# Performance work log

Measured on AMD Instinct MI355X. Metric: run time of the kernel, lower is better.

Reference implementation:

```python
import jax, jax.numpy as jnp
import numpy as np

B, S, C, H, L = 256, 8, 8, 501, 56


def _lin_init(k, out_dim, in_dim):
    k1, k2 = jax.random.split(k)
    s = 1.0 / np.sqrt(in_dim)
    w = jax.random.uniform(k1, (out_dim, in_dim), jnp.float32, -s, s)
    b = jax.random.uniform(k2, (out_dim,), jnp.float32, -s, s)
    return w, b


def setup_inputs() -> dict:
    key = jax.random.key(0)
    ks = jax.random.split(key, 12)
    lin1_w, lin1_b = _lin_init(ks[0], H, L)
    av_w1, av_b1 = _lin_init(ks[1], 2 * H, H)
    av_w2, av_b2 = _lin_init(ks[2], C, 2 * H)
    ae_w1, ae_b1 = _lin_init(ks[3], 4 * H, 2 * H)
    ae_w2, ae_b2 = _lin_init(ks[4], 1, 4 * H)
    gate_w, gate_b = _lin_init(ks[5], H, H)
    map_w, map_b = _lin_init(ks[6], H, H)
    gru_w_ih, gru_b_ih = _lin_init(ks[7], 3 * H, C)
    gru_w_hh, gru_b_hh = _lin_init(ks[8], 3 * H, H)
    z = jax.random.normal(ks[9], (B, L), jnp.float32)
    dep_graph = jax.random.uniform(ks[10], (B, S, S), jnp.float32)
    node_encoding = jax.random.uniform(ks[11], (B, S, C), jnp.float32)
    return dict(z=z, dep_graph=dep_graph, node_encoding=node_encoding,
                lin1_w=lin1_w, lin1_b=lin1_b,
                av_w1=av_w1, av_b1=av_b1, av_w2=av_w2, av_b2=av_b2,
                ae_w1=ae_w1, ae_b1=ae_b1, ae_w2=ae_w2, ae_b2=ae_b2,
                gate_w=gate_w, gate_b=gate_b, map_w=map_w, map_b=map_b,
                gru_w_ih=gru_w_ih, gru_w_hh=gru_w_hh,
                gru_b_ih=gru_b_ih, gru_b_hh=gru_b_hh)


def _forward(z, dep_graph, node_encoding,
             lin1_w, lin1_b, av_w1, av_b1, av_w2, av_b2,
             ae_w1, ae_b1, ae_w2, ae_b2, gate_w, gate_b, map_w, map_b,
             gru_w_ih, gru_w_hh, gru_b_ih, gru_b_hh):
    b, s, _ = dep_graph.shape
    h = lin1_w.shape[0]

    def gru(x, hid):  # torch GRUCell math
        gi = x @ gru_w_ih.T + gru_b_ih
        gh = hid @ gru_w_hh.T + gru_b_hh
        i_r, i_z, i_n = jnp.split(gi, 3, axis=-1)
        h_r, h_z, h_n = jnp.split(gh, 3, axis=-1)
        r = jax.nn.sigmoid(i_r + h_r)
        zz = jax.nn.sigmoid(i_z + h_z)
        n = jnp.tanh(i_n + r * h_n)
        return (1.0 - zz) * n + zz * hid

    pos = jnp.arange(s)

    def outer_step(carry, xs):
        graph_state, nhs = carry  # (B,H), (B,S,H)
        index, x, dep_row = xs    # scalar, (B,C), (B,S)
        logits = jax.nn.softmax(
            jax.nn.relu(graph_state @ av_w1.T + av_b1) @ av_w2.T + av_b2, axis=-1)
        # index==0: gru seeded with graph_state; otherwise zero hidden
        h0 = jnp.where(index == 0, graph_state, jnp.zeros_like(graph_state))
        hv0 = gru(x, h0)

        def inner_step(c, j):
            hv, nhs_c, edge_row = c
            active = j < index  # replicate range(index-1, -1, -1)
            hidden_j = nhs_c[:, j]
            e = jnp.concatenate([hv, hidden_j], axis=1)
            edge = (jax.nn.relu(e @ ae_w1.T + ae_b1) @ ae_w2.T + ae_b2)[:, 0]
            edge_row = edge_row.at[:, j].set(jnp.where(active, edge, 0.0))
            # ancestors: dep_graph[:, index] with positions < j zeroed
            anc = dep_row * (pos >= j).astype(dep_row.dtype)
            a = (nhs_c * anc[:, :, None]).reshape(b * s, h)
            h_in = (jax.nn.sigmoid(a @ gate_w.T + gate_b) *
                    (a @ map_w.T + map_b)).reshape(b, s, h).sum(axis=1)
            hv_new = gru(x, h_in)
            hv = jnp.where(active, hv_new, hv)
            nhs_c = nhs_c.at[:, index].set(jnp.where(active, hv_new, nhs_c[:, index]))
            return (hv, nhs_c, edge_row), None

        (hv, nhs, edge_row), _ = jax.lax.scan(
            inner_step, (hv0, nhs, jnp.zeros((b, s), dep_graph.dtype)),
            jnp.arange(s - 1, -1, -1))
        nhs = nhs.at[:, index].set(hv)
        return (hv, nhs), (logits, edge_row)

    graph_state0 = z @ lin1_w.T + lin1_b
    nhs0 = jnp.zeros((b, s, h), z.dtype)
    (_, _), (gen_enc, gen_dep) = jax.lax.scan(
        outer_step, (graph_state0, nhs0),
        (jnp.arange(s), node_encoding.transpose(1, 0, 2), dep_graph.transpose(1, 0, 2)))
    return gen_dep.transpose(1, 0, 2), gen_enc.transpose(1, 0, 2)


def reference(z, dep_graph, node_encoding,
              lin1_w, lin1_b, av_w1, av_b1, av_w2, av_b2,
              ae_w1, ae_b1, ae_w2, ae_b2, gate_w, gate_b, map_w, map_b,
              gru_w_ih, gru_w_hh, gru_b_ih, gru_b_hh):
    return _forward(z, dep_graph, node_encoding,
                    lin1_w, lin1_b, av_w1, av_b1, av_w2, av_b2,
                    ae_w1, ae_b1, ae_w2, ae_b2, gate_w, gate_b, map_w, map_b,
                    gru_w_ih, gru_w_hh, gru_b_ih, gru_b_hh)
```

## Files before the change

kernel.cpp:

```cpp
#include <hip/hip_runtime.h>
#include <math.h>

constexpr int NB  = 256;
constexpr int NS  = 8;
constexpr int NC  = 8;
constexpr int NH  = 501;
constexpr int NL  = 56;
constexpr int NH2 = 1002;
constexpr int NH3 = 1503;
constexpr int NH4 = 2004;
constexpr int KT  = 1536;
constexpr int KE  = 512;
constexpr int KA  = 1024;
constexpr int HV  = 512 * 256;

typedef unsigned short u16;
typedef short bf16x8v __attribute__((ext_vector_type(8)));
typedef _Float16 f16x8v __attribute__((ext_vector_type(8)));
typedef _Float16 f16x4v __attribute__((ext_vector_type(4)));
typedef float f32x4 __attribute__((ext_vector_type(4)));

__device__ __forceinline__ float sigf(float x) { return 1.0f / (1.0f + __expf(-x)); }
__device__ __forceinline__ float tanh2(float x) { return 2.0f * sigf(2.0f * x) - 1.0f; }

__device__ __forceinline__ u16 f2bf(float x) {
  union { float f; unsigned u; } c; c.f = x;
  unsigned r = (c.u + 0x7fffu + ((c.u >> 16) & 1u)) >> 16;
  return (u16)r;
}
__device__ __forceinline__ float bf2f(u16 h) {
  union { float f; unsigned u; } c; c.u = ((unsigned)h) << 16; return c.f;
}

__device__ __forceinline__ void async_copy16(const void* g, void* l) {
  __builtin_amdgcn_global_load_lds(
      (const __attribute__((address_space(1))) unsigned int*)g,
      (__attribute__((address_space(3))) unsigned int*)l, 16, 0, 0);
}

__device__ __forceinline__ f32x4 mfma_bf(bf16x8v a, bf16x8v b, f32x4 c) {
  return __builtin_amdgcn_mfma_f32_16x16x32_bf16(a, b, c, 0, 0, 0);
}
__device__ __forceinline__ f32x4 mfma_h(f16x8v a, f16x8v b, f32x4 c) {
  return __builtin_amdgcn_mfma_f32_16x16x32_f16(a, b, c, 0, 0, 0);
}

__device__ __forceinline__ void storeTrio(u16* __restrict__ T, int b, int h0, const float v[4]) {
  size_t base = (size_t)b * KT;
  if (h0 + 3 < NH) {
    ushort4 hi4, lo4;
    u16 hi, lo;
    hi = f2bf(v[0]); lo = f2bf(v[0] - bf2f(hi)); hi4.x = hi; lo4.x = lo;
    hi = f2bf(v[1]); lo = f2bf(v[1] - bf2f(hi)); hi4.y = hi; lo4.y = lo;
    hi = f2bf(v[2]); lo = f2bf(v[2] - bf2f(hi)); hi4.z = hi; lo4.z = lo;
    hi = f2bf(v[3]); lo = f2bf(v[3] - bf2f(hi)); hi4.w = hi; lo4.w = lo;
    *(ushort4*)&T[base + h0]        = hi4;
    *(ushort4*)&T[base + 512 + h0]  = lo4;
    *(ushort4*)&T[base + 1024 + h0] = hi4;
  } else {
    for (int r = 0; r < 4; ++r) {
      int h = h0 + r;
      if (h < NH) {
        u16 hi = f2bf(v[r]); u16 lo = f2bf(v[r] - bf2f(hi));
        T[base + h] = hi; T[base + 512 + h] = lo; T[base + 1024 + h] = hi;
      }
    }
  }
}

__global__ __launch_bounds__(256) void kPack(
    const float* __restrict__ gate_w, const float* __restrict__ map_w,
    const float* __restrict__ w_hh, const float* __restrict__ av_w1,
    const float* __restrict__ ae_w1,
    u16* __restrict__ Wgm, u16* __restrict__ Whh, u16* __restrict__ Wav1,
    _Float16* __restrict__ Wlr) {
  int r = blockIdx.x;
  if (r < 3584) {
    for (int k = threadIdx.x; k < 512; k += 256) {
      float v = 0.f; u16* dst; int rr;
      if (r < 1024) {
        int h = (r < 512) ? r : r - 512;
        if (h < NH && k < NH) v = (r < 512) ? gate_w[h * NH + k] : map_w[h * NH + k];
        dst = Wgm; rr = r;
      } else if (r < 2560) {
        rr = r - 1024; int g = rr >> 9, h = rr & 511;
        if (h < NH && k < NH) v = w_hh[((size_t)g * NH + h) * NH + k];
        dst = Whh;
      } else {
        rr = r - 2560;
        if (rr < NH2 && k < NH) v = av_w1[(size_t)rr * NH + k];
        dst = Wav1;
      }
      u16 hi = f2bf(v); u16 lo = f2bf(v - bf2f(hi));
      dst[(size_t)rr * KT + k] = hi;
      dst[(size_t)rr * KT + 512 + k] = hi;
      dst[(size_t)rr * KT + 1024 + k] = lo;
    }
  } else {
    int m = r - 3584;
    for (int k = threadIdx.x; k < KA; k += 256) {
      float v = 0.f;
      if (m < NH4) {
        if (k < 512) { if (k < NH) v = ae_w1[(size_t)m * NH2 + k]; }
        else { int kk = k - 512; if (kk < NH) v = ae_w1[(size_t)m * NH2 + NH + kk]; }
      }
      Wlr[(size_t)m * KA + k] = (_Float16)v;
    }
  }
}

__global__ __launch_bounds__(256) void kInit(
    float* __restrict__ out0, const float* __restrict__ ae_b2,
    u16* __restrict__ trio, _Float16* __restrict__ Xe, _Float16* __restrict__ Xn,
    const float* __restrict__ z, const float* __restrict__ lin1_w,
    const float* __restrict__ lin1_b, float* __restrict__ g0,
    const float* __restrict__ ne, const float* __restrict__ w_ih,
    const float* __restrict__ b_ih, float* __restrict__ giN, float* __restrict__ giT) {
  int blk = blockIdx.x, t = threadIdx.x;
  if (blk < 64) {
    int e = blk * 256 + t;
    int b = e >> 6, r = e & 63;
    int i = r >> 3, jj = r & 7;
    out0[b * 64 + i * 8 + jj] = (jj < i) ? ae_b2[0] : 0.f;
  } else if (blk < 75) {
    u16* T = trio + (size_t)(blk - 64) * ((size_t)NB * KT) + (size_t)t * KT;
#pragma unroll
    for (int seg = 0; seg < 3; ++seg)
      for (int h = NH; h < 512; ++h) T[seg * 512 + h] = 0;
  } else if (blk < 103) {
    _Float16* X = Xe + (size_t)(blk - 75) * NB * KE + (size_t)t * KE;
    for (int h = NH; h < 512; ++h) X[h] = (_Float16)0.f;
  } else if (blk < 110) {
    _Float16* X = Xn + (size_t)(blk - 103) * NB * KE + (size_t)t * KE;
    for (int h = NH; h < 512; ++h) X[h] = (_Float16)0.f;
  } else if (blk < 366) {
    int b = blk - 110;
    const float* zr = z + (size_t)b * NL;
    for (int h = t; h < NH; h += 256) {
      const float* wr = lin1_w + (size_t)h * NL;
      float acc = lin1_b[h];
#pragma unroll
      for (int l = 0; l < NL; ++l) acc += zr[l] * wr[l];
      g0[h * NB + b] = acc;
      u16 hi = f2bf(acc), lo = f2bf(acc - bf2f(hi));
      trio[(size_t)b * KT + h] = hi;
      trio[(size_t)b * KT + 512 + h] = lo;
      trio[(size_t)b * KT + 1024 + h] = hi;
    }
  } else {
    int r0 = (blk - 366) * 6, b = t;
    for (int rr = 0; rr < 6; ++rr) {
      int r = r0 + rr;
      if (r >= NH3) break;
      int g = (r >= NH2) ? 2 : ((r >= NH) ? 1 : 0);
      int h = r - g * NH;
      float wv[8];
#pragma unroll
      for (int c = 0; c < 8; ++c) wv[c] = w_ih[r * NC + c];
      float bb = b_ih[r];
      for (int idx = 0; idx < 8; ++idx) {
        float acc = bb;
#pragma unroll
        for (int c = 0; c < 8; ++c) acc += ne[b * 64 + idx * 8 + c] * wv[c];
        giN[((size_t)idx * NH3 + r) * NB + b] = acc;
        giT[((size_t)idx * NB + b) * KT + g * 512 + h] = acc;
      }
    }
  }
}


__global__ __launch_bounds__(256) void kGMT(
    const u16* __restrict__ Wgm, const u16* __restrict__ Bsrc,
    float* __restrict__ PcO, float* __restrict__ QcO,
    const float* __restrict__ dep, const float* __restrict__ gate_b,
    const float* __restrict__ map_b, float* __restrict__ RS, u16* __restrict__ hinT,
    const float* __restrict__ giT, const float* __restrict__ b_hh,
    _Float16* __restrict__ Xe0, int index) {
  __shared__ f32x4 red[4 * 4 * 64];
  const int b = blockIdx.x, t = threadIdx.x, w = t >> 6, l = t & 63;
  const int quad = l >> 4, lan = l & 15;
  const int ht = b & 31, ct = b >> 5;
  const u16* Ag = Wgm + (size_t)(ht * 16 + lan) * KT;
  const u16* Am = Wgm + (size_t)(512 + ht * 16 + lan) * KT;
  const u16* B0 = Bsrc + (size_t)(ct * 32 + lan) * KT;
  const u16* B1 = Bsrc + (size_t)(ct * 32 + 16 + lan) * KT;
  const int kb = w * 384 + quad * 8;
  f32x4 a0 = {0.f,0.f,0.f,0.f}, a1 = a0, a2 = a0, a3 = a0;
#pragma unroll 4
  for (int ks = 0; ks < 12; ++ks) {
    int k = kb + ks * 32;
    bf16x8v bg = *(const bf16x8v*)&B0[k];
    bf16x8v bh = *(const bf16x8v*)&B1[k];
    bf16x8v ag = *(const bf16x8v*)&Ag[k];
    bf16x8v am = *(const bf16x8v*)&Am[k];
    a0 = mfma_bf(ag, bg, a0); a1 = mfma_bf(ag, bh, a1);
    a2 = mfma_bf(am, bg, a2); a3 = mfma_bf(am, bh, a3);
  }
  red[(w * 4 + 0) * 64 + l] = a0;
  red[(w * 4 + 1) * 64 + l] = a1;
  red[(w * 4 + 2) * 64 + l] = a2;
  red[(w * 4 + 3) * 64 + l] = a3;
  __syncthreads();
  if (w < 2) {
    int ns = w;
    f32x4 G = red[(0 * 4 + ns) * 64 + l] + red[(1 * 4 + ns) * 64 + l] +
              red[(2 * 4 + ns) * 64 + l] + red[(3 * 4 + ns) * 64 + l];
    f32x4 M = red[(0 * 4 + 2 + ns) * 64 + l] + red[(1 * 4 + 2 + ns) * 64 + l] +
              red[(2 * 4 + 2 + ns) * 64 + l] + red[(3 * 4 + 2 + ns) * 64 + l];
    int c = ct * 32 + ns * 16 + lan;
    int h0 = ht * 16 + quad * 4;
    int j = index - 1;
    float dj = dep[c * 64 + index * 8 + j];
    float vout[4];
#pragma unroll
    for (int reg = 0; reg < 4; ++reg) {
      int h = h0 + reg; float v = 0.f;
      if (h < NH) {
        PcO[h * NB + c] = G[reg];
        QcO[h * NB + c] = M[reg];
        float gb = gate_b[h], mb = map_b[h];
        float kbv = sigf(gb) * mb;
        float fj = sigf(dj * G[reg] + gb) * (dj * M[reg] + mb);
        RS[h * NB + c] = fj;
        v = fj + 7.0f * kbv;
      }
      vout[reg] = v;
    }
    storeTrio(hinT, c, h0, vout);
  } else {
    int t2 = t - 128;
    int c = ct * 32 + (t2 & 31);
    int hb = t2 >> 5;
    const float* g = giT + ((size_t)index * NB + c) * KT;
#pragma unroll
    for (int k = 0; k < 4; ++k) {
      int h = ht * 16 + hb * 4 + k;
      if (h < NH) {
        float rr = sigf(g[h] + b_hh[h]);
        float zz = sigf(g[512 + h] + b_hh[NH + h]);
        float nn = tanh2(g[1024 + h] + rr * b_hh[2 * NH + h]);
        Xe0[(size_t)c * KE + h] = (_Float16)((1.f - zz) * nn);
      }
    }
  }
}

__global__ __launch_bounds__(256) void kGM0(
    const u16* __restrict__ Wgm, const u16* __restrict__ Bsrc,
    const float* __restrict__ dep, const float* __restrict__ gate_b,
    const float* __restrict__ map_b,
    const float* __restrict__ Pcj, const float* __restrict__ Qcj,
    float* __restrict__ RS, u16* __restrict__ hinT, int index, int j) {
  __shared__ f32x4 red[4 * 4 * 64];
  const int b = blockIdx.x, t = threadIdx.x, w = t >> 6, l = t & 63;
  const int quad = l >> 4, lan = l & 15;
  const int ht = b & 31, ct = b >> 5;
  const u16* Ag = Wgm + (size_t)(ht * 16 + lan) * KT;
  const u16* Am = Wgm + (size_t)(512 + ht * 16 + lan) * KT;
  const u16* B0 = Bsrc + (size_t)(ct * 32 + lan) * KT;
  const u16* B1 = Bsrc + (size_t)(ct * 32 + 16 + lan) * KT;
  const int kb = w * 384 + quad * 8;
  f32x4 a0 = {0.f,0.f,0.f,0.f}, a1 = a0, a2 = a0, a3 = a0;
#pragma unroll 4
  for (int ks = 0; ks < 12; ++ks) {
    int k = kb + ks * 32;
    bf16x8v bg = *(const bf16x8v*)&B0[k];
    bf16x8v bh = *(const bf16x8v*)&B1[k];
    bf16x8v ag = *(const bf16x8v*)&Ag[k];
    bf16x8v am = *(const bf16x8v*)&Am[k];
    a0 = mfma_bf(ag, bg, a0); a1 = mfma_bf(ag, bh, a1);
    a2 = mfma_bf(am, bg, a2); a3 = mfma_bf(am, bh, a3);
  }
  red[(w * 4 + 0) * 64 + l] = a0;
  red[(w * 4 + 1) * 64 + l] = a1;
  red[(w * 4 + 2) * 64 + l] = a2;
  red[(w * 4 + 3) * 64 + l] = a3;
  __syncthreads();
  if (w < 2) {
    int ns = w;
    f32x4 G = red[(0 * 4 + ns) * 64 + l] + red[(1 * 4 + ns) * 64 + l] +
              red[(2 * 4 + ns) * 64 + l] + red[(3 * 4 + ns) * 64 + l];
    f32x4 M = red[(0 * 4 + 2 + ns) * 64 + l] + red[(1 * 4 + 2 + ns) * 64 + l] +
              red[(2 * 4 + 2 + ns) * 64 + l] + red[(3 * 4 + 2 + ns) * 64 + l];
    int c = ct * 32 + ns * 16 + lan;
    int h0 = ht * 16 + quad * 4;
    float dj = dep[c * 64 + index * 8 + j];
    float di = dep[c * 64 + index * 8 + index];
    float cnt = (float)(7 - (index - j));
    float vout[4];
#pragma unroll
    for (int reg = 0; reg < 4; ++reg) {
      int h = h0 + reg; float v = 0.f;
      if (h < NH) {
        float gb = gate_b[h], mb = map_b[h];
        float kbv = sigf(gb) * mb;
        float fj = sigf(dj * Pcj[h * NB + c] + gb) * (dj * Qcj[h * NB + c] + mb);
        float rs = RS[h * NB + c] + fj;
        RS[h * NB + c] = rs;
        float fi = sigf(di * G[reg] + gb) * (di * M[reg] + mb);
        v = rs + fi + cnt * kbv;
      }
      vout[reg] = v;
    }
    storeTrio(hinT, c, h0, vout);
  }
}

__global__ __launch_bounds__(256) void kHHw(
    const u16* __restrict__ Whh, const u16* __restrict__ Bsrc,
    const float* __restrict__ hidF, const float* __restrict__ gi,
    const float* __restrict__ b_hh,
    u16* __restrict__ dstT, _Float16* __restrict__ XeSlot, _Float16* __restrict__ XnSlot) {
  __shared__ f32x4 red[4 * 6 * 64];
  const int b = blockIdx.x, t = threadIdx.x, w = t >> 6, l = t & 63;
  const int quad = l >> 4, lan = l & 15;
  const int ht = b & 31, ct = b >> 5;
  const u16* Ar = Whh + (size_t)(ht * 16 + lan) * KT;
  const u16* Az = Whh + (size_t)(512 + ht * 16 + lan) * KT;
  const u16* An = Whh + (size_t)(1024 + ht * 16 + lan) * KT;
  const u16* B0 = Bsrc + (size_t)(ct * 32 + lan) * KT;
  const u16* B1 = Bsrc + (size_t)(ct * 32 + 16 + lan) * KT;
  const int kb = w * 384 + quad * 8;
  f32x4 r0 = {0.f,0.f,0.f,0.f}, r1 = r0, z0 = r0, z1 = r0, n0 = r0, n1 = r0;
#pragma unroll 4
  for (int ks = 0; ks < 12; ++ks) {
    int k = kb + ks * 32;
    bf16x8v bg = *(const bf16x8v*)&B0[k];
    bf16x8v bh = *(const bf16x8v*)&B1[k];
    bf16x8v ar = *(const bf16x8v*)&Ar[k];
    bf16x8v az = *(const bf16x8v*)&Az[k];
    bf16x8v an = *(const bf16x8v*)&An[k];
    r0 = mfma_bf(ar, bg, r0); r1 = mfma_bf(ar, bh, r1);
    z0 = mfma_bf(az, bg, z0); z1 = mfma_bf(az, bh, z1);
    n0 = mfma_bf(an, bg, n0); n1 = mfma_bf(an, bh, n1);
  }
  red[(w * 6 + 0) * 64 + l] = r0;
  red[(w * 6 + 1) * 64 + l] = r1;
  red[(w * 6 + 2) * 64 + l] = z0;
  red[(w * 6 + 3) * 64 + l] = z1;
  red[(w * 6 + 4) * 64 + l] = n0;
  red[(w * 6 + 5) * 64 + l] = n1;
  __syncthreads();
  if (w < 2) {
    int ns = w;
    f32x4 Rr = red[(0 * 6 + 0 + ns) * 64 + l] + red[(1 * 6 + 0 + ns) * 64 + l] +
               red[(2 * 6 + 0 + ns) * 64 + l] + red[(3 * 6 + 0 + ns) * 64 + l];
    f32x4 Rz = red[(0 * 6 + 2 + ns) * 64 + l] + red[(1 * 6 + 2 + ns) * 64 + l] +
               red[(2 * 6 + 2 + ns) * 64 + l] + red[(3 * 6 + 2 + ns) * 64 + l];
    f32x4 Rn = red[(0 * 6 + 4 + ns) * 64 + l] + red[(1 * 6 + 4 + ns) * 64 + l] +
               red[(2 * 6 + 4 + ns) * 64 + l] + red[(3 * 6 + 4 + ns) * 64 + l];
    int c = ct * 32 + ns * 16 + lan;
    int h0 = ht * 16 + quad * 4;
    float vout[4];
#pragma unroll
    for (int reg = 0; reg < 4; ++reg) {
      int h = h0 + reg; float v = 0.f;
      if (h < NH) {
        float ir = gi[h * NB + c];
        float iz = gi[(NH + h) * NB + c];
        float inn = gi[(2 * NH + h) * NB + c];
        float rr = sigf(ir + Rr[reg] + b_hh[h]);
        float zz = sigf(iz + Rz[reg] + b_hh[NH + h]);
        float nn = tanh2(inn + rr * (Rn[reg] + b_hh[2 * NH + h]));
        float hd;
        if (hidF) hd = hidF[h * NB + c];
        else hd = bf2f(Bsrc[(size_t)c * KT + h]) + bf2f(Bsrc[(size_t)c * KT + 512 + h]);
        v = (1.f - zz) * nn + zz * hd;
      }
      vout[reg] = v;
    }
    storeTrio(dstT, c, h0, vout);
    if (XeSlot || XnSlot) {
      if (h0 + 3 < NH) {
        f16x4v xv; xv[0] = (_Float16)vout[0]; xv[1] = (_Float16)vout[1];
        xv[2] = (_Float16)vout[2]; xv[3] = (_Float16)vout[3];
        if (XeSlot) *(f16x4v*)&XeSlot[(size_t)c * KE + h0] = xv;
        if (XnSlot) *(f16x4v*)&XnSlot[(size_t)c * KE + h0] = xv;
      } else {
        for (int reg = 0; reg < 4; ++reg)
          if (h0 + reg < NH) {
            if (XeSlot) XeSlot[(size_t)c * KE + h0 + reg] = (_Float16)vout[reg];
            if (XnSlot) XnSlot[(size_t)c * KE + h0 + reg] = (_Float16)vout[reg];
          }
      }
    }
  }
}


__global__ __launch_bounds__(256) void kEdge(const _Float16* __restrict__ Wlr,
                                             const _Float16* __restrict__ Xe,
                                             const _Float16* __restrict__ Xn,
                                             const float* __restrict__ ae_b1,
                                             const float* __restrict__ ae_w2,
                                             float* __restrict__ out0) {
  __shared__ u16 sA[2][128 * 32];
  __shared__ u16 sB[2][128 * 32];
  __shared__ float shW[4][8][16];
  const int t = threadIdx.x, w = t >> 6, l = t & 63, quad = l >> 4, lan = l & 15;
  const int mB = blockIdx.x * 128, nB0 = blockIdx.y * 128;
  const int qs = quad ^ ((lan >> 1) & 3);
  const int sseg = (l & 3) ^ ((l >> 3) & 3);
  int sid = blockIdx.y >> 1;
  int idec = 1, bse = 0;
  while (sid >= bse + idec) { bse += idec; idec++; }
  int jdec = idec - 1 - (sid - bse);
  int r0 = (w * 2 + 0) * 16 + (l >> 2), r1 = (w * 2 + 1) * 16 + (l >> 2);
  const _Float16* gA0 = Wlr + (size_t)(mB + r0) * KA + sseg * 8;
  const _Float16* gA1 = Wlr + (size_t)(mB + r1) * KA + sseg * 8;
  const _Float16* Xe0 = Xe + (size_t)(nB0 + r0) * KE + sseg * 8;
  const _Float16* Xe1 = Xe + (size_t)(nB0 + r1) * KE + sseg * 8;
  const _Float16* Xn0 = Xn + ((size_t)jdec * NB + ((nB0 + r0) & 255)) * KE + sseg * 8;
  const _Float16* Xn1 = Xn + ((size_t)jdec * NB + ((nB0 + r1) & 255)) * KE + sseg * 8;
  f32x4 acc[2][8];
#pragma unroll
  for (int mt = 0; mt < 2; ++mt)
#pragma unroll
    for (int ns = 0; ns < 8; ++ns) acc[mt][ns] = (f32x4){0.f,0.f,0.f,0.f};
  async_copy16(gA0, &sA[0][(w * 2 + 0) * 512]);
  async_copy16(gA1, &sA[0][(w * 2 + 1) * 512]);
  async_copy16(Xe0, &sB[0][(w * 2 + 0) * 512]);
  async_copy16(Xe1, &sB[0][(w * 2 + 1) * 512]);
  for (int c = 0; c < 32; ++c) {
    __syncthreads();
    if (c + 1 < 32) {
      int nb = (c + 1) & 1, cc = c + 1;
      async_copy16(gA0 + cc * 32, &sA[nb][(w * 2 + 0) * 512]);
      async_copy16(gA1 + cc * 32, &sA[nb][(w * 2 + 1) * 512]);
      const _Float16* b0 = (cc < 16) ? (Xe0 + cc * 32) : (Xn0 + (cc - 16) * 32);
      const _Float16* b1 = (cc < 16) ? (Xe1 + cc * 32) : (Xn1 + (cc - 16) * 32);
      async_copy16(b0, &sB[nb][(w * 2 + 0) * 512]);
      async_copy16(b1, &sB[nb][(w * 2 + 1) * 512]);
    }
    const u16* bufA = sA[c & 1];
    const u16* bufB = sB[c & 1];
    f16x8v av[2];
#pragma unroll
    for (int mt = 0; mt < 2; ++mt)
      av[mt] = *(const f16x8v*)&bufA[(w * 32 + mt * 16 + lan) * 32 + qs * 8];
#pragma unroll
    for (int ns = 0; ns < 8; ++ns) {
      f16x8v bv = *(const f16x8v*)&bufB[(ns * 16 + lan) * 32 + qs * 8];
#pragma unroll
      for (int mt = 0; mt < 2; ++mt) acc[mt][ns] = mfma_h(av[mt], bv, acc[mt][ns]);
    }
  }
  float b1v[2][4], w2v[2][4];
#pragma unroll
  for (int mt = 0; mt < 2; ++mt) {
    int m0 = mB + w * 32 + mt * 16 + quad * 4;
#pragma unroll
    for (int reg = 0; reg < 4; ++reg) {
      int m = m0 + reg;
      b1v[mt][reg] = (m < NH4) ? ae_b1[m] : 0.f;
      w2v[mt][reg] = (m < NH4) ? ae_w2[m] : 0.f;
    }
  }
#pragma unroll
  for (int ns = 0; ns < 8; ++ns) {
    float s = 0.f;
#pragma unroll
    for (int mt = 0; mt < 2; ++mt) {
#pragma unroll
      for (int reg = 0; reg < 4; ++reg) {
        float v = acc[mt][ns][reg] + b1v[mt][reg];
        if (v > 0.f) s += v * w2v[mt][reg];
      }
    }
    s += __shfl_xor(s, 16);
    s += __shfl_xor(s, 32);
    if (quad == 0) shW[w][ns][lan] = s;
  }
  __syncthreads();
  if (t < 128) {
    int ns = t >> 4, ln = t & 15;
    float tot = shW[0][ns][ln] + shW[1][ns][ln] + shW[2][ns][ln] + shW[3][ns][ln];
    int b = (nB0 + ln + ns * 16) & 255;
    atomicAdd(&out0[b * 64 + idec * 8 + jdec], tot);
  }
}

__global__ __launch_bounds__(256) void kLogA(const u16* __restrict__ Wav1,
                                             const u16* __restrict__ Bsrc,
                                             const float* __restrict__ av_b1,
                                             _Float16* __restrict__ t1) {
  __shared__ u16 sA[2][64 * 32];
  __shared__ u16 sB[2][128 * 32];
  const int t = threadIdx.x, w = t >> 6, l = t & 63, quad = l >> 4, lan = l & 15;
  const int mB = blockIdx.x * 64, nB0 = blockIdx.y * 128;
  const int qs = quad ^ ((lan >> 1) & 3);
  const int sseg = (l & 3) ^ ((l >> 3) & 3);
  int rA = w * 16 + (l >> 2);
  int r0 = (w * 2 + 0) * 16 + (l >> 2), r1 = (w * 2 + 1) * 16 + (l >> 2);
  const u16* gA = Wav1 + (size_t)(mB + rA) * KT + sseg * 8;
  const u16* gB0 = Bsrc + (size_t)(nB0 + r0) * KT + sseg * 8;
  const u16* gB1 = Bsrc + (size_t)(nB0 + r1) * KT + sseg * 8;
  f32x4 acc[8];
#pragma unroll
  for (int ns = 0; ns < 8; ++ns) acc[ns] = (f32x4){0.f,0.f,0.f,0.f};
  async_copy16(gA, &sA[0][w * 512]);
  async_copy16(gB0, &sB[0][(w * 2 + 0) * 512]);
  async_copy16(gB1, &sB[0][(w * 2 + 1) * 512]);
  for (int c = 0; c < 48; ++c) {
    __syncthreads();
    if (c + 1 < 48) {
      int nb = (c + 1) & 1, off = (c + 1) * 32;
      async_copy16(gA + off, &sA[nb][w * 512]);
      async_copy16(gB0 + off, &sB[nb][(w * 2 + 0) * 512]);
      async_copy16(gB1 + off, &sB[nb][(w * 2 + 1) * 512]);
    }
    const u16* bufA = sA[c & 1];
    const u16* bufB = sB[c & 1];
    bf16x8v av = *(const bf16x8v*)&bufA[(w * 16 + lan) * 32 + qs * 8];
#pragma unroll
    for (int ns = 0; ns < 8; ++ns) {
      bf16x8v bv = *(const bf16x8v*)&bufB[(ns * 16 + lan) * 32 + qs * 8];
      acc[ns] = mfma_bf(av, bv, acc[ns]);
    }
  }
#pragma unroll
  for (int ns = 0; ns < 8; ++ns) {
    int col = nB0 + ns * 16 + lan;
    int m0 = mB + w * 16 + quad * 4;
    f16x4v rv;
#pragma unroll
    for (int reg = 0; reg < 4; ++reg) {
      int m = m0 + reg;
      float v = acc[ns][reg] + ((m < NH2) ? av_b1[m] : 0.f);
      rv[reg] = (_Float16)(v > 0.f ? v : 0.f);
    }
    *(f16x4v*)&t1[(size_t)col * 1024 + m0] = rv;
  }
}

__global__ __launch_bounds__(256) void kSoft(const _Float16* __restrict__ t1,
                                             const float* __restrict__ av_w2,
                                             const float* __restrict__ av_b2,
                                             float* __restrict__ out1) {
  const int t = threadIdx.x, w = t >> 6, l = t & 63;
  int col = blockIdx.x * 4 + w;
  const _Float16* trow = t1 + (size_t)col * 1024;
  float s[8] = {};
  for (int i = 0; i < 16; ++i) {
    int k = i * 64 + l;
    if (k < NH2) {
      float v = (float)trow[k];
#pragma unroll
      for (int c = 0; c < 8; ++c) s[c] += v * av_w2[c * NH2 + k];
    }
  }
#pragma unroll
  for (int c = 0; c < 8; ++c) {
    s[c] += __shfl_xor(s[c], 32);
    s[c] += __shfl_xor(s[c], 16);
    s[c] += __shfl_xor(s[c], 8);
    s[c] += __shfl_xor(s[c], 4);
    s[c] += __shfl_xor(s[c], 2);
    s[c] += __shfl_xor(s[c], 1);
  }
  if (l == 0) {
    float lg[8], mx = -1e30f;
#pragma unroll
    for (int c = 0; c < 8; ++c) { lg[c] = s[c] + av_b2[c]; mx = fmaxf(mx, lg[c]); }
    float den = 0.f;
#pragma unroll
    for (int c = 0; c < 8; ++c) den += __expf(lg[c] - mx);
    int idx = col >> 8, b = col & 255;
#pragma unroll
    for (int c = 0; c < 8; ++c)
      out1[(b * NS + idx) * NC + c] = __expf(lg[c] - mx) / den;
  }
}


extern "C" void kernel_launch(void* const* d_in, const int* in_sizes, int n_in,
                              void* d_out, int out_size, void* d_ws, size_t ws_size,
                              hipStream_t stream) {
  (void)in_sizes; (void)n_in; (void)out_size; (void)ws_size;
  const float* z      = (const float*)d_in[0];
  const float* dep    = (const float*)d_in[1];
  const float* ne     = (const float*)d_in[2];
  const float* lin1_w = (const float*)d_in[3];
  const float* lin1_b = (const float*)d_in[4];
  const float* av_w1  = (const float*)d_in[5];
  const float* av_b1  = (const float*)d_in[6];
  const float* av_w2  = (const float*)d_in[7];
  const float* av_b2  = (const float*)d_in[8];
  const float* ae_w1  = (const float*)d_in[9];
  const float* ae_b1  = (const float*)d_in[10];
  const float* ae_w2  = (const float*)d_in[11];
  const float* ae_b2  = (const float*)d_in[12];
  const float* gate_w = (const float*)d_in[13];
  const float* gate_b = (const float*)d_in[14];
  const float* map_w  = (const float*)d_in[15];
  const float* map_b  = (const float*)d_in[16];
  const float* w_ih   = (const float*)d_in[17];
  const float* w_hh   = (const float*)d_in[18];
  const float* b_ih   = (const float*)d_in[19];
  const float* b_hh   = (const float*)d_in[20];

  float* out0 = (float*)d_out;
  float* out1 = out0 + NB * NS * NS;

  const size_t SLOT = (size_t)NB * KT;
  char* p = (char*)d_ws;
  u16* trio = (u16*)p;            p += 11 * SLOT * 2;
  _Float16* Xe = (_Float16*)p;    p += (size_t)28 * NB * KE * 2;
  _Float16* Xn = (_Float16*)p;    p += (size_t)7 * NB * KE * 2;
  u16* Wgm  = (u16*)p;            p += (size_t)1024 * KT * 2;
  u16* Whh  = (u16*)p;            p += (size_t)1536 * KT * 2;
  u16* Wav1 = (u16*)p;            p += (size_t)1024 * KT * 2;
  _Float16* Wlr = (_Float16*)p;   p += (size_t)2048 * KA * 2;
  _Float16* t1 = (_Float16*)p;    p += (size_t)2048 * 1024 * 2;
  float* Pc   = (float*)p;        p += (size_t)8 * HV * 4;
  float* Qc   = (float*)p;        p += (size_t)8 * HV * 4;
  float* RS   = (float*)p;        p += (size_t)HV * 4;
  float* g0   = (float*)p;        p += (size_t)HV * 4;
  float* giN  = (float*)p;        p += (size_t)8 * NH3 * NB * 4;
  float* giT  = (float*)p;        p += (size_t)8 * NB * KT * 4;

  u16* hinT = trio + 8 * SLOT;

  kPack<<<5632, 256, 0, stream>>>(gate_w, map_w, w_hh, av_w1, ae_w1, Wgm, Whh, Wav1, Wlr);
  kInit<<<617, 256, 0, stream>>>(out0, ae_b2, trio, Xe, Xn,
                                 z, lin1_w, lin1_b, g0, ne, w_ih, b_ih, giN, giT);

  kHHw<<<256, 256, 0, stream>>>(Whh, trio, g0, giN, b_hh,
                                trio + 1 * SLOT, nullptr, Xn);

  for (int i = 0; i <= 6; ++i) {
    int index = i + 1;
    int sid0 = index * (index - 1) / 2;
    const float* gi_i = giN + (size_t)index * NH3 * NB;
    kGMT<<<256, 256, 0, stream>>>(Wgm, trio + (size_t)(i + 1) * SLOT,
                                  Pc + (size_t)i * HV, Qc + (size_t)i * HV,
                                  dep, gate_b, map_b, RS, hinT, giT, b_hh,
                                  Xe + (size_t)sid0 * NB * KE, index);
    bool final1 = (index == 1);
    u16* dst = final1 ? (trio + 2 * SLOT) : (trio + 9 * SLOT);
    kHHw<<<256, 256, 0, stream>>>(Whh, hinT, nullptr, gi_i, b_hh, dst,
        (index - 1 > 0) ? (Xe + (size_t)(sid0 + 1) * NB * KE) : nullptr,
        final1 ? (Xn + (size_t)1 * NB * KE) : nullptr);
    u16* prev = dst;
    int par = 1;
    for (int j = index - 2; j >= 0; --j) {
      kGM0<<<256, 256, 0, stream>>>(Wgm, prev, dep, gate_b, map_b,
                                    Pc + (size_t)j * HV, Qc + (size_t)j * HV,
                                    RS, hinT, index, j);
      bool fin = (j == 0);
      u16* d2 = (fin && index <= 6) ? (trio + (size_t)(index + 1) * SLOT)
                                    : (trio + (size_t)(9 + par) * SLOT);
      kHHw<<<256, 256, 0, stream>>>(Whh, hinT, nullptr, gi_i, b_hh, d2,
          (j > 0) ? (Xe + (size_t)(sid0 + index - j) * NB * KE) : nullptr,
          (fin && index <= 6) ? (Xn + (size_t)index * NB * KE) : nullptr);
      prev = d2; par ^= 1;
    }
  }

  kLogA<<<dim3(16, 16), 256, 0, stream>>>(Wav1, trio, av_b1, t1);
  kSoft<<<512, 256, 0, stream>>>(t1, av_w2, av_b2, out1);
  kEdge<<<dim3(16, 56), 256, 0, stream>>>(Wlr, Xe, Xn, ae_b1, ae_w2, out0);
}
```

Baseline: 886.1 us.

## Fuse recurrent GMT/GM0/HH launch chain into one cooperative persistent kernel

Replaces the roughly 57 sequential small kernel launches of the recurrent loop with one cooperative kernel of 256 blocks that runs each phase and separates them with grid-wide syncs. This removes per-launch overhead and the inter-kernel gaps on the serial dependency chain. The cost is a grid barrier per phase. All phases now share the larger shared-memory reduction buffer, which may slightly affect occupancy. Correctness depends on all 256 blocks being co-resident, which the cooperative launch requires.

```diff
diff --git a/kernel.cpp b/kernel.cpp
--- a/kernel.cpp
+++ b/kernel.cpp
@@ -1,5 +1,8 @@
 #include <hip/hip_runtime.h>
+#include <hip/hip_cooperative_groups.h>
 #include <math.h>
+
+namespace cg = cooperative_groups;
 
 constexpr int NB  = 256;
 constexpr int NS  = 8;
@@ -13,6 +16,7 @@
 constexpr int KE  = 512;
 constexpr int KA  = 1024;
 constexpr int HV  = 512 * 256;
+constexpr size_t SLOT = (size_t)NB * KT;
 
 typedef unsigned short u16;
 typedef short bf16x8v __attribute__((ext_vector_type(8)));
@@ -170,14 +174,13 @@
 }
 
 
-__global__ __launch_bounds__(256) void kGMT(
+__device__ __forceinline__ void phase_gmt(
     const u16* __restrict__ Wgm, const u16* __restrict__ Bsrc,
     float* __restrict__ PcO, float* __restrict__ QcO,
     const float* __restrict__ dep, const float* __restrict__ gate_b,
     const float* __restrict__ map_b, float* __restrict__ RS, u16* __restrict__ hinT,
     const float* __restrict__ giT, const float* __restrict__ b_hh,
-    _Float16* __restrict__ Xe0, int index) {
-  __shared__ f32x4 red[4 * 4 * 64];
+    _Float16* __restrict__ Xe0, int index, f32x4* red) {
   const int b = blockIdx.x, t = threadIdx.x, w = t >> 6, l = t & 63;
   const int quad = l >> 4, lan = l & 15;
   const int ht = b & 31, ct = b >> 5;
@@ -246,13 +249,12 @@
   }
 }
 
-__global__ __launch_bounds__(256) void kGM0(
+__device__ __forceinline__ void phase_gm0(
     const u16* __restrict__ Wgm, const u16* __restrict__ Bsrc,
     const float* __restrict__ dep, const float* __restrict__ gate_b,
     const float* __restrict__ map_b,
     const float* __restrict__ Pcj, const float* __restrict__ Qcj,
-    float* __restrict__ RS, u16* __restrict__ hinT, int index, int j) {
-  __shared__ f32x4 red[4 * 4 * 64];
+    float* __restrict__ RS, u16* __restrict__ hinT, int index, int j, f32x4* red) {
   const int b = blockIdx.x, t = threadIdx.x, w = t >> 6, l = t & 63;
   const int quad = l >> 4, lan = l & 15;
   const int ht = b & 31, ct = b >> 5;
@@ -307,12 +309,12 @@
   }
 }
 
-__global__ __launch_bounds__(256) void kHHw(
+__device__ __forceinline__ void phase_hh(
     const u16* __restrict__ Whh, const u16* __restrict__ Bsrc,
     const float* __restrict__ hidF, const float* __restrict__ gi,
     const float* __restrict__ b_hh,
-    u16* __restrict__ dstT, _Float16* __restrict__ XeSlot, _Float16* __restrict__ XnSlot) {
-  __shared__ f32x4 red[4 * 6 * 64];
+    u16* __restrict__ dstT, _Float16* __restrict__ XeSlot, _Float16* __restrict__ XnSlot,
+    f32x4* red) {
   const int b = blockIdx.x, t = threadIdx.x, w = t >> 6, l = t & 63;
   const int quad = l >> 4, lan = l & 15;
   const int ht = b & 31, ct = b >> 5;
@@ -384,6 +386,57 @@
             if (XnSlot) XnSlot[(size_t)c * KE + h0 + reg] = (_Float16)vout[reg];
           }
       }
+    }
+  }
+}
+
+__global__ __launch_bounds__(256) void kLoop(
+    const u16* __restrict__ Wgm, const u16* __restrict__ Whh,
+    u16* __restrict__ trio, u16* __restrict__ hinT,
+    const float* __restrict__ dep, const float* __restrict__ gate_b,
+    const float* __restrict__ map_b,
+    float* __restrict__ Pc, float* __restrict__ Qc, float* __restrict__ RS,
+    const float* __restrict__ giT, const float* __restrict__ giN,
+    const float* __restrict__ g0, const float* __restrict__ b_hh,
+    _Float16* __restrict__ Xe, _Float16* __restrict__ Xn) {
+  cg::grid_group grid = cg::this_grid();
+  __shared__ f32x4 red[4 * 6 * 64];
+
+  phase_hh(Whh, trio, g0, giN, b_hh, trio + SLOT, nullptr, Xn, red);
+  grid.sync();
+
+  for (int index = 1; index <= 7; ++index) {
+    const int i = index - 1;
+    const int sid0 = index * (index - 1) / 2;
+    const float* gi_i = giN + (size_t)index * NH3 * NB;
+
+    phase_gmt(Wgm, trio + (size_t)index * SLOT,
+              Pc + (size_t)i * HV, Qc + (size_t)i * HV,
+              dep, gate_b, map_b, RS, hinT, giT, b_hh,
+              Xe + (size_t)sid0 * NB * KE, index, red);
+    grid.sync();
+
+    const bool final1 = (index == 1);
+    u16* dst = final1 ? (trio + 2 * SLOT) : (trio + 9 * SLOT);
+    phase_hh(Whh, hinT, nullptr, gi_i, b_hh, dst,
+             (index - 1 > 0) ? (Xe + (size_t)(sid0 + 1) * NB * KE) : nullptr,
+             final1 ? (Xn + (size_t)1 * NB * KE) : nullptr, red);
+    grid.sync();
+
+    const u16* prev = dst;
+    int par = 1;
+    for (int j = index - 2; j >= 0; --j) {
+      phase_gm0(Wgm, prev, dep, gate_b, map_b,
+                Pc + (size_t)j * HV, Qc + (size_t)j * HV, RS, hinT, index, j, red);
+      grid.sync();
+      const bool fin = (j == 0);
+      u16* d2 = (fin && index <= 6) ? (trio + (size_t)(index + 1) * SLOT)
+                                    : (trio + (size_t)(9 + par) * SLOT);
+      phase_hh(Whh, hinT, nullptr, gi_i, b_hh, d2,
+               (j > 0) ? (Xe + (size_t)(sid0 + index - j) * NB * KE) : nullptr,
+               (fin && index <= 6) ? (Xn + (size_t)index * NB * KE) : nullptr, red);
+      grid.sync();
+      prev = d2; par ^= 1;
     }
   }
 }
@@ -603,7 +656,6 @@
   float* out0 = (float*)d_out;
   float* out1 = out0 + NB * NS * NS;
 
-  const size_t SLOT = (size_t)NB * KT;
   char* p = (char*)d_ws;
   u16* trio = (u16*)p;            p += 11 * SLOT * 2;
   _Float16* Xe = (_Float16*)p;    p += (size_t)28 * NB * KE * 2;
@@ -626,36 +678,15 @@
   kInit<<<617, 256, 0, stream>>>(out0, ae_b2, trio, Xe, Xn,
                                  z, lin1_w, lin1_b, g0, ne, w_ih, b_ih, giN, giT);
 
-  kHHw<<<256, 256, 0, stream>>>(Whh, trio, g0, giN, b_hh,
-                                trio + 1 * SLOT, nullptr, Xn);
-
-  for (int i = 0; i <= 6; ++i) {
-    int index = i + 1;
-    int sid0 = index * (index - 1) / 2;
-    const float* gi_i = giN + (size_t)index * NH3 * NB;
-    kGMT<<<256, 256, 0, stream>>>(Wgm, trio + (size_t)(i + 1) * SLOT,
-                                  Pc + (size_t)i * HV, Qc + (size_t)i * HV,
-                                  dep, gate_b, map_b, RS, hinT, giT, b_hh,
-                                  Xe + (size_t)sid0 * NB * KE, index);
-    bool final1 = (index == 1);
-    u16* dst = final1 ? (trio + 2 * SLOT) : (trio + 9 * SLOT);
-    kHHw<<<256, 256, 0, stream>>>(Whh, hinT, nullptr, gi_i, b_hh, dst,
-        (index - 1 > 0) ? (Xe + (size_t)(sid0 + 1) * NB * KE) : nullptr,
-        final1 ? (Xn + (size_t)1 * NB * KE) : nullptr);
-    u16* prev = dst;
-    int par = 1;
-    for (int j = index - 2; j >= 0; --j) {
-      kGM0<<<256, 256, 0, stream>>>(Wgm, prev, dep, gate_b, map_b,
-                                    Pc + (size_t)j * HV, Qc + (size_t)j * HV,
-                                    RS, hinT, index, j);
-      bool fin = (j == 0);
-      u16* d2 = (fin && index <= 6) ? (trio + (size_t)(index + 1) * SLOT)
-                                    : (trio + (size_t)(9 + par) * SLOT);
-      kHHw<<<256, 256, 0, stream>>>(Whh, hinT, nullptr, gi_i, b_hh, d2,
-          (j > 0) ? (Xe + (size_t)(sid0 + index - j) * NB * KE) : nullptr,
-          (fin && index <= 6) ? (Xn + (size_t)index * NB * KE) : nullptr);
-      prev = d2; par ^= 1;
-    }
+  {
+    void* kargs[] = {
+      (void*)&Wgm, (void*)&Whh, (void*)&trio, (void*)&hinT,
+      (void*)&dep, (void*)&gate_b, (void*)&map_b,
+      (void*)&Pc, (void*)&Qc, (void*)&RS,
+      (void*)&giT, (void*)&giN, (void*)&g0, (void*)&b_hh,
+      (void*)&Xe, (void*)&Xn
+    };
+    hipLaunchCooperativeKernel((void*)kLoop, dim3(256), dim3(256), kargs, 0, stream);
   }
 
   kLogA<<<dim3(16, 16), 256, 0, stream>>>(Wav1, trio, av_b1, t1);
```

Result: slower. 2.629 ms (+196.8%).
